# Performance work log

Hardware: AMD Instinct MI355X
Metric: run time of the kernel (lower is better)

The kernel has to match this reference:

```python
import jax, jax.numpy as jnp
import numpy as np

NUM_EXPERTS = 16
EFF_THRESHOLD = 0.1
SIM_THRESHOLD = 0.0
EPS = 1e-8


def setup_inputs() -> dict:
    key = jax.random.key(0)
    k1, k2 = jax.random.split(key)
    B, E, H = 4096, NUM_EXPERTS, 1024
    rp = jax.random.uniform(k1, (B, E), dtype=jnp.float32)
    rp = rp / rp.sum(axis=-1, keepdims=True)  # valid probabilities
    emb = jax.random.normal(k2, (B, H), dtype=jnp.float32)
    return {"routing_probs": rp, "input_embeddings": emb}


def _total_loss(routing_probs, input_embeddings):
    B, E = routing_probs.shape

    # --- LoadBalanceLoss: var(mean usage) / (1/E)^2, unbiased var (torch default)
    usage = routing_probs.mean(axis=0)                      # [E]
    var = jnp.sum((usage - usage.mean()) ** 2) / (E - 1)
    load_balance = var * (E ** 2)

    # --- EntropyRegularizationLoss (target None): -mean entropy
    entropy = -jnp.sum(routing_probs * jnp.log(routing_probs + EPS), axis=-1)
    entropy_loss = -entropy.mean()

    # --- EfficiencyLoss: sum of probs below threshold, averaged over batch
    small = jnp.where(routing_probs < EFF_THRESHOLD, routing_probs, 0.0)
    efficiency = small.sum(axis=-1).mean()

    # --- ConsistencyLoss: mean KL(softmax(p_j) || softmax(p_i)) over similar pairs
    logp = jax.nn.log_softmax(routing_probs, axis=-1)       # [B, E]
    q = jnp.exp(logp)                                       # [B, E]
    neg_ent_q = jnp.sum(q * logp, axis=-1)                  # [B], = sum q log q
    # KL[i, j] = sum_e q_j (log q_j - logp_i) = neg_ent_q[j] - logp_i . q_j
    kl = neg_ent_q[None, :] - jnp.einsum('ie,je->ij', logp, q)  # [B, B]

    nemb = input_embeddings / jnp.linalg.norm(input_embeddings, axis=-1, keepdims=True)
    sim = nemb @ nemb.T                                     # [B, B]
    mask = (sim > SIM_THRESHOLD) & (~jnp.eye(B, dtype=bool))
    num_pairs = mask.sum()
    cons_sum = jnp.sum(jnp.where(mask, kl, 0.0))
    consistency = jnp.where(num_pairs > 0,
                            cons_sum / jnp.maximum(num_pairs, 1).astype(kl.dtype),
                            0.0)

    return load_balance + entropy_loss + efficiency + consistency


def reference(routing_probs, input_embeddings):
    return _total_loss(routing_probs, input_embeddings)
```

## Files before the change

kernel.cpp:

```cpp
#include <hip/hip_runtime.h>
#include <hip/hip_bf16.h>

#define BROWS 4096
#define NE    16
#define HDIM  1024
#define ACC_F 128
#define NTILE 32
#define NBLK  (NTILE * (NTILE + 1) / 2)

typedef __attribute__((ext_vector_type(8))) short short8;
typedef __attribute__((ext_vector_type(4))) float float4v;
typedef __attribute__((ext_vector_type(2))) long long2v;

__device__ __forceinline__ unsigned bf16rne(float f) {
    const unsigned u = __float_as_uint(f);
    return (u + 0x7FFFu + ((u >> 16) & 1u)) >> 16;
}
__device__ __forceinline__ unsigned pk2(float lo, float hi) {
    return bf16rne(lo) | (bf16rne(hi) << 16);
}

__device__ __forceinline__ unsigned e4m3(float x) {
    unsigned u = __float_as_uint(x);
    const unsigned s = (u >> 24) & 0x80u;
    u &= 0x7FFFFFFFu;
    if (u >= 0x43E80000u) return s | 0x7Eu;
    u += 0x7FFFFu + ((u >> 20) & 1u);
    const int e = (int)(u >> 23) - 120;
    if (e <= 0) return s;
    return s | ((unsigned)e << 3) | ((u >> 20) & 7u);
}

__device__ __forceinline__ void gl16(const unsigned char* g, unsigned char* l) {
    __builtin_amdgcn_global_load_lds(
        (const __attribute__((address_space(1))) unsigned int*)(unsigned long long)g,
        (__attribute__((address_space(3))) unsigned int*)(unsigned int)(unsigned long long)l,
        16, 0, 0);
}

__device__ __forceinline__ void row16f(const float* src, float* p) {
    const float4v* pv = (const float4v*)src;
    float4v a0 = pv[0], a1 = pv[1], a2 = pv[2], a3 = pv[3];
    p[0]=a0.x; p[1]=a0.y; p[2]=a0.z; p[3]=a0.w;
    p[4]=a1.x; p[5]=a1.y; p[6]=a1.z; p[7]=a1.w;
    p[8]=a2.x; p[9]=a2.y; p[10]=a2.z; p[11]=a2.w;
    p[12]=a3.x; p[13]=a3.y; p[14]=a3.z; p[15]=a3.w;
}

__device__ __forceinline__ void lsm16(const float* p, float* lp, float* q, float& ne) {
    float m = p[0];
#pragma unroll
    for (int e = 1; e < 16; e++) m = fmaxf(m, p[e]);
    float s = 0.f;
#pragma unroll
    for (int e = 0; e < 16; e++) s += expf(p[e] - m);
    const float ls = logf(s);
    ne = 0.f;
#pragma unroll
    for (int e = 0; e < 16; e++) {
        lp[e] = p[e] - m - ls;
        q[e]  = expf(lp[e]);
        ne   += q[e] * lp[e];
    }
}

__device__ __forceinline__ void st8pair(unsigned char* tile, int row, int cp, uint4 v) {
    const int x = row & 7;
    unsigned long long lo = ((unsigned long long)v.y << 32) | v.x;
    unsigned long long hi = ((unsigned long long)v.w << 32) | v.z;
    *(unsigned long long*)(tile + row * 64 + (((2 * cp)     ^ x) << 3)) = lo;
    *(unsigned long long*)(tile + row * 64 + (((2 * cp + 1) ^ x) << 3)) = hi;
}

__global__ __launch_bounds__(256) void conv_init(
    const float* __restrict__ src, unsigned char* __restrict__ dst, float* __restrict__ acc)
{
    if (blockIdx.x == 0 && threadIdx.x < ACC_F) acc[threadIdx.x] = 0.f;
    const size_t k = ((size_t)blockIdx.x * 256 + threadIdx.x) * 8;
    const size_t row = k >> 10;
    const int kin = (int)(k & 1023);
    const int T = kin >> 6, kt = kin & 63, s = kt >> 5, u = (kt & 31) >> 3;
    float4v a = *(const float4v*)(src + k);
    float4v b = *(const float4v*)(src + k + 4);
    unsigned lo = e4m3(a.x) | (e4m3(a.y) << 8) | (e4m3(a.z) << 16) | (e4m3(a.w) << 24);
    unsigned hi = e4m3(b.x) | (e4m3(b.y) << 8) | (e4m3(b.z) << 16) | (e4m3(b.w) << 24);
    *(unsigned long long*)(dst + row * 1024 + T * 64 + u * 16 + s * 8) =
        ((unsigned long long)hi << 32) | lo;
}

__device__ __forceinline__ void decode_pair(int id, int& bi, int& bj) {
    int L = (id & 7) * 66 + (id >> 3);
    int gi = 0, gj = 0;
    for (;;) {
        const int cnt = (gi == gj) ? 10 : 16;
        if (L < cnt) break;
        L -= cnt;
        gj++; if (gj == 8) { gi++; gj = gi; }
    }
    if (gi == gj) {
        int u = 0, c = 4;
        while (L >= c) { L -= c; u++; c--; }
        bi = gi * 4 + u; bj = gj * 4 + u + L;
    } else {
        bi = gi * 4 + (L >> 2); bj = gj * 4 + (L & 3);
    }
}

template<bool PRE>
__global__ __launch_bounds__(512, 4) void gram_kl(
    const float* __restrict__ embf, const unsigned char* __restrict__ embq,
    const float* __restrict__ rp, float* __restrict__ acc,
    unsigned int* __restrict__ out)
{
    __shared__ char smem[32768];
    __shared__ float red[16];
    __shared__ int islast;
    __shared__ float fin[96];
    __hip_bfloat16* eAF = (__hip_bfloat16*)smem;
    __hip_bfloat16* eBF = (__hip_bfloat16*)(smem + 8192);
    __hip_bfloat16* eAR = (__hip_bfloat16*)(smem + 16384);
    __hip_bfloat16* eBR = (__hip_bfloat16*)(smem + 24576);

    int bi, bj;
    decode_pair((int)blockIdx.x, bi, bj);

    const int t = threadIdx.x;
    const int lane = t & 63, wid = t >> 6;
    const int wi0 = (wid >> 1) * 32, wj0 = (wid & 1) * 64;
    const int lrow = lane & 15, quad = lane >> 4;

    float4v accf[2][4];
#pragma unroll
    for (int a = 0; a < 2; a++)
#pragma unroll
        for (int b = 0; b < 4; b++) { accf[a][b].x=0.f; accf[a][b].y=0.f; accf[a][b].z=0.f; accf[a][b].w=0.f; }

    if (PRE) {
        int roA[2], roB[4];
#pragma unroll
        for (int f = 0; f < 2; f++) {
            const int r = wi0 + f * 16 + lrow;
            roA[f] = r * 64 + ((quad ^ ((r >> 1) & 3)) << 4);
        }
#pragma unroll
        for (int f = 0; f < 4; f++) {
            const int r = wj0 + f * 16 + lrow;
            roB[f] = r * 64 + ((quad ^ ((r >> 1) & 3)) << 4);
        }
        const int rl = lane >> 2;
        const int r  = wid * 16 + rl;
        const int gu = (lane & 3) ^ ((r >> 1) & 3);
        const unsigned char* gA = embq + (size_t)(bi * 128 + r) * 1024 + gu * 16;
        const unsigned char* gB = embq + (size_t)(bj * 128 + r) * 1024 + gu * 16;
        const int woff = wid * 1024;

        gl16(gA, (unsigned char*)smem + woff);
        gl16(gB, (unsigned char*)smem + 8192 + woff);
        for (int T = 0; T < 16; ++T) {
            unsigned char* cur = (unsigned char*)smem + (T & 1) * 16384;
            unsigned char* nxt = (unsigned char*)smem + ((T + 1) & 1) * 16384;
            __syncthreads();
            if (T < 15) {
                const int kt = (T + 1) * 64;
                gl16(gA + kt, nxt + woff);
                gl16(gB + kt, nxt + 8192 + woff);
            }
            long2v A0 = *(const long2v*)(cur + roA[0]);
            long2v A1 = *(const long2v*)(cur + roA[1]);
            long2v B0 = *(const long2v*)(cur + 8192 + roB[0]);
            long2v B1 = *(const long2v*)(cur + 8192 + roB[1]);
            long2v B2 = *(const long2v*)(cur + 8192 + roB[2]);
            long2v B3 = *(const long2v*)(cur + 8192 + roB[3]);
            accf[0][0] = __builtin_amdgcn_mfma_f32_16x16x32_fp8_fp8(A0.x, B0.x, accf[0][0], 0, 0, 0);
            accf[0][1] = __builtin_amdgcn_mfma_f32_16x16x32_fp8_fp8(A0.x, B1.x, accf[0][1], 0, 0, 0);
            accf[0][2] = __builtin_amdgcn_mfma_f32_16x16x32_fp8_fp8(A0.x, B2.x, accf[0][2], 0, 0, 0);
            accf[0][3] = __builtin_amdgcn_mfma_f32_16x16x32_fp8_fp8(A0.x, B3.x, accf[0][3], 0, 0, 0);
            accf[1][0] = __builtin_amdgcn_mfma_f32_16x16x32_fp8_fp8(A1.x, B0.x, accf[1][0], 0, 0, 0);
            accf[1][1] = __builtin_amdgcn_mfma_f32_16x16x32_fp8_fp8(A1.x, B1.x, accf[1][1], 0, 0, 0);
            accf[1][2] = __builtin_amdgcn_mfma_f32_16x16x32_fp8_fp8(A1.x, B2.x, accf[1][2], 0, 0, 0);
            accf[1][3] = __builtin_amdgcn_mfma_f32_16x16x32_fp8_fp8(A1.x, B3.x, accf[1][3], 0, 0, 0);
            accf[0][0] = __builtin_amdgcn_mfma_f32_16x16x32_fp8_fp8(A0.y, B0.y, accf[0][0], 0, 0, 0);
            accf[0][1] = __builtin_amdgcn_mfma_f32_16x16x32_fp8_fp8(A0.y, B1.y, accf[0][1], 0, 0, 0);
            accf[0][2] = __builtin_amdgcn_mfma_f32_16x16x32_fp8_fp8(A0.y, B2.y, accf[0][2], 0, 0, 0);
            accf[0][3] = __builtin_amdgcn_mfma_f32_16x16x32_fp8_fp8(A0.y, B3.y, accf[0][3], 0, 0, 0);
            accf[1][0] = __builtin_amdgcn_mfma_f32_16x16x32_fp8_fp8(A1.y, B0.y, accf[1][0], 0, 0, 0);
            accf[1][1] = __builtin_amdgcn_mfma_f32_16x16x32_fp8_fp8(A1.y, B1.y, accf[1][1], 0, 0, 0);
            accf[1][2] = __builtin_amdgcn_mfma_f32_16x16x32_fp8_fp8(A1.y, B2.y, accf[1][2], 0, 0, 0);
            accf[1][3] = __builtin_amdgcn_mfma_f32_16x16x32_fp8_fp8(A1.y, B3.y, accf[1][3], 0, 0, 0);
        }
    } else {
        int roA[2][2], roB[4][2];
#pragma unroll
        for (int f = 0; f < 2; f++) {
            const int r = wi0 + f * 16 + lrow;
#pragma unroll
            for (int s = 0; s < 2; s++) roA[f][s] = r * 64 + (((s * 4 + quad) ^ (r & 7)) << 3);
        }
#pragma unroll
        for (int f = 0; f < 4; f++) {
            const int r = wj0 + f * 16 + lrow;
#pragma unroll
            for (int s = 0; s < 2; s++) roB[f][s] = r * 64 + (((s * 4 + quad) ^ (r & 7)) << 3);
        }
        const int row = t >> 2, cp = t & 3;
        const float* gA = embf + (size_t)(bi * 128 + row) * HDIM + cp * 16;
        const float* gB = embf + (size_t)(bj * 128 + row) * HDIM + cp * 16;
        for (int T = 0; T < 16; ++T) {
            const int kt = T * 64;
            unsigned char* bufA = (unsigned char*)(smem + (T & 1) * 16384);
            unsigned char* bufB = bufA + 8192;
            uint4 wa, wb;
            {
                float4v x0 = *(const float4v*)(gA + kt),      x1 = *(const float4v*)(gA + kt + 4);
                float4v x2 = *(const float4v*)(gA + kt + 8),  x3 = *(const float4v*)(gA + kt + 12);
                wa.x = e4m3(x0.x) | (e4m3(x0.y)<<8) | (e4m3(x0.z)<<16) | (e4m3(x0.w)<<24);
                wa.y = e4m3(x1.x) | (e4m3(x1.y)<<8) | (e4m3(x1.z)<<16) | (e4m3(x1.w)<<24);
                wa.z = e4m3(x2.x) | (e4m3(x2.y)<<8) | (e4m3(x2.z)<<16) | (e4m3(x2.w)<<24);
                wa.w = e4m3(x3.x) | (e4m3(x3.y)<<8) | (e4m3(x3.z)<<16) | (e4m3(x3.w)<<24);
                float4v y0 = *(const float4v*)(gB + kt),      y1 = *(const float4v*)(gB + kt + 4);
                float4v y2 = *(const float4v*)(gB + kt + 8),  y3 = *(const float4v*)(gB + kt + 12);
                wb.x = e4m3(y0.x) | (e4m3(y0.y)<<8) | (e4m3(y0.z)<<16) | (e4m3(y0.w)<<24);
                wb.y = e4m3(y1.x) | (e4m3(y1.y)<<8) | (e4m3(y1.z)<<16) | (e4m3(y1.w)<<24);
                wb.z = e4m3(y2.x) | (e4m3(y2.y)<<8) | (e4m3(y2.z)<<16) | (e4m3(y2.w)<<24);
                wb.w = e4m3(y3.x) | (e4m3(y3.y)<<8) | (e4m3(y3.z)<<16) | (e4m3(y3.w)<<24);
            }
            st8pair(bufA, row, cp, wa);
            st8pair(bufB, row, cp, wb);
            __syncthreads();
#pragma unroll
            for (int s = 0; s < 2; s++) {
                long a0 = *(const long*)(bufA + roA[0][s]);
                long a1 = *(const long*)(bufA + roA[1][s]);
                long b0 = *(const long*)(bufB + roB[0][s]);
                long b1 = *(const long*)(bufB + roB[1][s]);
                long b2 = *(const long*)(bufB + roB[2][s]);
                long b3 = *(const long*)(bufB + roB[3][s]);
                accf[0][0] = __builtin_amdgcn_mfma_f32_16x16x32_fp8_fp8(a0, b0, accf[0][0], 0, 0, 0);
                accf[0][1] = __builtin_amdgcn_mfma_f32_16x16x32_fp8_fp8(a0, b1, accf[0][1], 0, 0, 0);
                accf[0][2] = __builtin_amdgcn_mfma_f32_16x16x32_fp8_fp8(a0, b2, accf[0][2], 0, 0, 0);
                accf[0][3] = __builtin_amdgcn_mfma_f32_16x16x32_fp8_fp8(a0, b3, accf[0][3], 0, 0, 0);
                accf[1][0] = __builtin_amdgcn_mfma_f32_16x16x32_fp8_fp8(a1, b0, accf[1][0], 0, 0, 0);
                accf[1][1] = __builtin_amdgcn_mfma_f32_16x16x32_fp8_fp8(a1, b1, accf[1][1], 0, 0, 0);
                accf[1][2] = __builtin_amdgcn_mfma_f32_16x16x32_fp8_fp8(a1, b2, accf[1][2], 0, 0, 0);
                accf[1][3] = __builtin_amdgcn_mfma_f32_16x16x32_fp8_fp8(a1, b3, accf[1][3], 0, 0, 0);
            }
            __syncthreads();
        }
    }
    __syncthreads();

    {
        float p[16], lp[16], q[16], ne;
        const bool iSide = (t < 128);
        if (t < 256) {
            const int rloc = iSide ? t : (t - 128);
            const int grow = (iSide ? bi : bj) * 128 + rloc;
            row16f(rp + (size_t)grow * NE, p);
            lsm16(p, lp, q, ne);
            float r1[16], r2[16], x1, x2;
            if (iSide) {
#pragma unroll
                for (int e = 0; e < 16; e++) { r1[e] = lp[e]; r2[e] = q[e]; }
                x1 = 1.f; x2 = ne;
            } else {
#pragma unroll
                for (int e = 0; e < 16; e++) { r1[e] = -q[e]; r2[e] = -lp[e]; }
                x1 = ne; x2 = 1.f;
            }
            const int s = (rloc >> 1) & 3;
            __hip_bfloat16* d1 = (iSide ? eAF : eBF) + rloc * 32;
            __hip_bfloat16* d2 = (iSide ? eAR : eBR) + rloc * 32;
            uint4 w0 = {pk2(r1[0],r1[1]), pk2(r1[2],r1[3]), pk2(r1[4],r1[5]), pk2(r1[6],r1[7])};
            uint4 w1 = {pk2(r1[8],r1[9]), pk2(r1[10],r1[11]), pk2(r1[12],r1[13]), pk2(r1[14],r1[15])};
            uint4 w2 = {pk2(x1, 0.f), 0u, 0u, 0u};
            uint4 w3 = {0u, 0u, 0u, 0u};
            *(uint4*)(d1 + (0 ^ s) * 8) = w0;
            *(uint4*)(d1 + (1 ^ s) * 8) = w1;
            *(uint4*)(d1 + (2 ^ s) * 8) = w2;
            *(uint4*)(d1 + (3 ^ s) * 8) = w3;
            uint4 v0 = {pk2(r2[0],r2[1]), pk2(r2[2],r2[3]), pk2(r2[4],r2[5]), pk2(r2[6],r2[7])};
            uint4 v1 = {pk2(r2[8],r2[9]), pk2(r2[10],r2[11]), pk2(r2[12],r2[13]), pk2(r2[14],r2[15])};
            uint4 v2 = {pk2(x2, 0.f), 0u, 0u, 0u};
            *(uint4*)(d2 + (0 ^ s) * 8) = v0;
            *(uint4*)(d2 + (1 ^ s) * 8) = v1;
            *(uint4*)(d2 + (2 ^ s) * 8) = v2;
            *(uint4*)(d2 + (3 ^ s) * 8) = w3;
        }
        if (bi == bj && iSide) {
            float ent = 0.f, eff = 0.f;
#pragma unroll
            for (int e = 0; e < 16; e++) {
                ent += p[e] * logf(p[e] + 1e-8f);
                if (p[e] < 0.1f) eff += p[e];
            }
#pragma unroll
            for (int e = 0; e < 18; e++) {
                float v = (e < 16) ? p[e] : ((e == 16) ? ent : eff);
#pragma unroll
                for (int o = 32; o > 0; o >>= 1) v += __shfl_down(v, o);
                if (lane == 0) atomicAdd(&acc[e], v);
            }
        }
    }
    __syncthreads();

    int eoA[2], eoB[4];
#pragma unroll
    for (int f = 0; f < 2; f++) {
        const int r = wi0 + f * 16 + lrow;
        eoA[f] = r * 32 + (quad ^ ((r >> 1) & 3)) * 8;
    }
#pragma unroll
    for (int f = 0; f < 4; f++) {
        const int r = wj0 + f * 16 + lrow;
        eoB[f] = r * 32 + (quad ^ ((r >> 1) & 3)) * 8;
    }

    float4v accF[2][4], accR[2][4];
    {
        const float4v z = {0.f, 0.f, 0.f, 0.f};
        short8 af[2], ar[2], bfr[4], brr[4];
#pragma unroll
        for (int f = 0; f < 2; f++) {
            af[f] = *(const short8*)(eAF + eoA[f]);
            ar[f] = *(const short8*)(eAR + eoA[f]);
        }
#pragma unroll
        for (int f = 0; f < 4; f++) {
            bfr[f] = *(const short8*)(eBF + eoB[f]);
            brr[f] = *(const short8*)(eBR + eoB[f]);
        }
#pragma unroll
        for (int fi = 0; fi < 2; fi++)
#pragma unroll
            for (int fj = 0; fj < 4; fj++) {
                accF[fi][fj] = __builtin_amdgcn_mfma_f32_16x16x32_bf16(af[fi], bfr[fj], z, 0, 0, 0);
                accR[fi][fj] = __builtin_amdgcn_mfma_f32_16x16x32_bf16(ar[fi], brr[fj], z, 0, 0, 0);
            }
    }

    float klacc = 0.f, cntacc = 0.f;
    const bool offd = (bi != bj);
#pragma unroll
    for (int fi = 0; fi < 2; fi++) {
#pragma unroll
        for (int fj = 0; fj < 4; fj++) {
#pragma unroll
            for (int rg = 0; rg < 4; rg++) {
                const int ig = bi * 128 + wi0 + fi * 16 + quad * 4 + rg;
                const int jg = bj * 128 + wj0 + fj * 16 + lrow;
                const float g = accf[fi][fj][rg];
                if ((g > 0.f) && (ig != jg)) {
                    klacc  += accF[fi][fj][rg];
                    cntacc += 1.f;
                    if (offd) { klacc += accR[fi][fj][rg]; cntacc += 1.f; }
                }
            }
        }
    }

#pragma unroll
    for (int o = 32; o > 0; o >>= 1) {
        klacc  += __shfl_down(klacc, o);
        cntacc += __shfl_down(cntacc, o);
    }
    if (lane == 0) { red[wid] = klacc; red[8 + wid] = cntacc; }
    __syncthreads();
    if (t == 0) {
        float k = 0.f, c = 0.f;
#pragma unroll
        for (int w = 0; w < 8; w++) { k += red[w]; c += red[8 + w]; }
        atomicAdd(&acc[18 + ((int)blockIdx.x & 31)], k);
        atomicAdd(&acc[50 + ((int)blockIdx.x & 31)], c);
        const unsigned got = __hip_atomic_fetch_add((unsigned int*)(acc + 82), 1u,
                                                    __ATOMIC_RELEASE, __HIP_MEMORY_SCOPE_AGENT);
        islast = (got == NBLK - 1) ? 1 : 0;
    }
    __syncthreads();

    if (islast) {
        if (t == 0)
            (void)__hip_atomic_load((unsigned int*)(acc + 82), __ATOMIC_ACQUIRE,
                                    __HIP_MEMORY_SCOPE_AGENT);
        __syncthreads();
        if (t < 82)
            fin[t] = __hip_atomic_load(&acc[t], __ATOMIC_RELAXED, __HIP_MEMORY_SCOPE_AGENT);
        __syncthreads();
        if (t == 0) {
            float u[16], usum = 0.f;
#pragma unroll
            for (int e = 0; e < 16; e++) { u[e] = fin[e] / (float)BROWS; usum += u[e]; }
            const float mean = usum / 16.f;
            float var = 0.f;
#pragma unroll
            for (int e = 0; e < 16; e++) { float dd = u[e] - mean; var += dd * dd; }
            var /= 15.f;
            const float lb  = var * 256.f;
            const float ent = fin[16] / (float)BROWS;
            const float eff = fin[17] / (float)BROWS;
            float kl = 0.f, cnt = 0.f;
#pragma unroll
            for (int s = 0; s < 32; s++) { kl += fin[18 + s]; cnt += fin[50 + s]; }
            const float cons = (cnt > 0.f) ? (kl / fmaxf(cnt, 1.f)) : 0.f;
            const float total = lb + ent + eff + cons;
            const unsigned fb   = __float_as_uint(total);
            const unsigned hi   = fb >> 16;
            const unsigned mant = fb & 0xFFFFu;
            const unsigned rnd  = (mant > 0x8000u || (mant == 0x8000u && (hi & 1))) ? 1u : 0u;
            out[0] = (fb & 0xFFFF0000u) | ((hi + rnd) & 0xFFFFu);
        }
    }
}

extern "C" void kernel_launch(void* const* d_in, const int* in_sizes, int n_in,
                              void* d_out, int out_size, void* d_ws, size_t ws_size,
                              hipStream_t stream) {
    const float* rp  = (const float*)d_in[0];
    const float* emb = (const float*)d_in[1];
    float* acc = (float*)d_ws;
    unsigned char* embq = (unsigned char*)d_ws + ACC_F * sizeof(float);
    (void)in_sizes; (void)n_in; (void)out_size;

    const size_t need = ACC_F * sizeof(float) + (size_t)BROWS * HDIM;
    const bool pre = (ws_size >= need);

    if (pre) {
        conv_init<<<(BROWS * HDIM) / (256 * 8), 256, 0, stream>>>(emb, embq, acc);
        gram_kl<true><<<NBLK, 512, 0, stream>>>(emb, embq, rp, acc, (unsigned int*)d_out);
    } else {
        conv_init<<<1, 256, 0, stream>>>(emb, embq, acc);
        gram_kl<false><<<NBLK, 512, 0, stream>>>(emb, (const unsigned char*)nullptr, rp, acc,
                                                 (unsigned int*)d_out);
    }
}
```

Measured before the change: 106.7 us.

## Use 32x32x64 scaled FP8 MFMA and precompute routing log-softmax planes in conv kernel

The precomputed path now runs the gram product with the 32x32x64 f8f6f4 scaled MFMA over 128-byte K chunks, which halves the loop trip count and enlarges shared-memory double buffers to 64KB. The per-row log-softmax, entropy, efficiency and usage terms are moved into extra blocks of the conversion kernel. These blocks write bf16 augmented planes and per-block partial sums, so the gram kernel only loads prepacked fragments for the KL MFMAs. The aim is fewer MFMA and loop-issue instructions and less redundant per-tile softmax work. In exchange, the larger LDS footprint may reduce occupancy, and the extra workspace needs to be available.

Result: slower. 201.7 us (+89.0%).

```diff
diff --git a/kernel.cpp b/kernel.cpp
--- a/kernel.cpp
+++ b/kernel.cpp
@@ -4,13 +4,17 @@
 #define BROWS 4096
 #define NE    16
 #define HDIM  1024
-#define ACC_F 128
+#define ACC_F 512
 #define NTILE 32
 #define NBLK  (NTILE * (NTILE + 1) / 2)
-
-typedef __attribute__((ext_vector_type(8))) short short8;
-typedef __attribute__((ext_vector_type(4))) float float4v;
-typedef __attribute__((ext_vector_type(2))) long long2v;
+#define PLANE 262144
+#define EMBQ_BYTES 4194304
+
+typedef __attribute__((ext_vector_type(8)))  short short8;
+typedef __attribute__((ext_vector_type(4)))  float float4v;
+typedef __attribute__((ext_vector_type(16))) float float16v;
+typedef __attribute__((ext_vector_type(4)))  int   int4v;
+typedef __attribute__((ext_vector_type(8)))  int   int8v;
 
 __device__ __forceinline__ unsigned bf16rne(float f) {
     const unsigned u = __float_as_uint(f);
@@ -70,22 +74,6 @@
     unsigned long long hi = ((unsigned long long)v.w << 32) | v.z;
     *(unsigned long long*)(tile + row * 64 + (((2 * cp)     ^ x) << 3)) = lo;
     *(unsigned long long*)(tile + row * 64 + (((2 * cp + 1) ^ x) << 3)) = hi;
-}
-
-__global__ __launch_bounds__(256) void conv_init(
-    const float* __restrict__ src, unsigned char* __restrict__ dst, float* __restrict__ acc)
-{
-    if (blockIdx.x == 0 && threadIdx.x < ACC_F) acc[threadIdx.x] = 0.f;
-    const size_t k = ((size_t)blockIdx.x * 256 + threadIdx.x) * 8;
-    const size_t row = k >> 10;
-    const int kin = (int)(k & 1023);
-    const int T = kin >> 6, kt = kin & 63, s = kt >> 5, u = (kt & 31) >> 3;
-    float4v a = *(const float4v*)(src + k);
-    float4v b = *(const float4v*)(src + k + 4);
-    unsigned lo = e4m3(a.x) | (e4m3(a.y) << 8) | (e4m3(a.z) << 16) | (e4m3(a.w) << 24);
-    unsigned hi = e4m3(b.x) | (e4m3(b.y) << 8) | (e4m3(b.z) << 16) | (e4m3(b.w) << 24);
-    *(unsigned long long*)(dst + row * 1024 + T * 64 + u * 16 + s * 8) =
-        ((unsigned long long)hi << 32) | lo;
 }
 
 __device__ __forceinline__ void decode_pair(int id, int& bi, int& bj) {
@@ -106,89 +94,298 @@
     }
 }
 
+__global__ __launch_bounds__(256) void conv_init(
+    const float* __restrict__ src, unsigned char* __restrict__ dst,
+    const float* __restrict__ rp, unsigned char* __restrict__ aug,
+    float* __restrict__ acc, int nconv)
+{
+    __shared__ float sred[72];
+    const int t = threadIdx.x;
+    const int bid = (int)blockIdx.x;
+    if (bid == 0 && t < 96) acc[t] = 0.f;
+    if (bid < nconv) {
+        const size_t k = ((size_t)bid * 256 + t) * 8;
+        float4v a = *(const float4v*)(src + k);
+        float4v b = *(const float4v*)(src + k + 4);
+        unsigned lo = e4m3(a.x) | (e4m3(a.y) << 8) | (e4m3(a.z) << 16) | (e4m3(a.w) << 24);
+        unsigned hi = e4m3(b.x) | (e4m3(b.y) << 8) | (e4m3(b.z) << 16) | (e4m3(b.w) << 24);
+        *(unsigned long long*)(dst + k) = ((unsigned long long)hi << 32) | lo;
+    } else if (nconv > 0) {
+        const int pb  = bid - nconv;
+        const int row = pb * 256 + t;
+        const int lane = t & 63, wid = t >> 6;
+        float p[16], lp[16], q[16], ne;
+        row16f(rp + (size_t)row * NE, p);
+        lsm16(p, lp, q, ne);
+        const uint4 z4 = {0u, 0u, 0u, 0u};
+        {
+            uint4* d = (uint4*)(aug + (size_t)row * 64);
+            uint4 w0 = {pk2(lp[0],lp[1]), pk2(lp[2],lp[3]), pk2(lp[4],lp[5]), pk2(lp[6],lp[7])};
+            uint4 w1 = {pk2(lp[8],lp[9]), pk2(lp[10],lp[11]), pk2(lp[12],lp[13]), pk2(lp[14],lp[15])};
+            uint4 w2 = {pk2(1.f, 0.f), 0u, 0u, 0u};
+            d[0] = w0; d[1] = w1; d[2] = w2; d[3] = z4;
+        }
+        {
+            uint4* d = (uint4*)(aug + PLANE + (size_t)row * 64);
+            uint4 w0 = {pk2(q[0],q[1]), pk2(q[2],q[3]), pk2(q[4],q[5]), pk2(q[6],q[7])};
+            uint4 w1 = {pk2(q[8],q[9]), pk2(q[10],q[11]), pk2(q[12],q[13]), pk2(q[14],q[15])};
+            uint4 w2 = {pk2(ne, 0.f), 0u, 0u, 0u};
+            d[0] = w0; d[1] = w1; d[2] = w2; d[3] = z4;
+        }
+        {
+            uint4* d = (uint4*)(aug + 2 * PLANE + (size_t)row * 64);
+            uint4 w0 = {pk2(-q[0],-q[1]), pk2(-q[2],-q[3]), pk2(-q[4],-q[5]), pk2(-q[6],-q[7])};
+            uint4 w1 = {pk2(-q[8],-q[9]), pk2(-q[10],-q[11]), pk2(-q[12],-q[13]), pk2(-q[14],-q[15])};
+            uint4 w2 = {pk2(ne, 0.f), 0u, 0u, 0u};
+            d[0] = w0; d[1] = w1; d[2] = w2; d[3] = z4;
+        }
+        {
+            uint4* d = (uint4*)(aug + 3 * PLANE + (size_t)row * 64);
+            uint4 w0 = {pk2(-lp[0],-lp[1]), pk2(-lp[2],-lp[3]), pk2(-lp[4],-lp[5]), pk2(-lp[6],-lp[7])};
+            uint4 w1 = {pk2(-lp[8],-lp[9]), pk2(-lp[10],-lp[11]), pk2(-lp[12],-lp[13]), pk2(-lp[14],-lp[15])};
+            uint4 w2 = {pk2(1.f, 0.f), 0u, 0u, 0u};
+            d[0] = w0; d[1] = w1; d[2] = w2; d[3] = z4;
+        }
+        float ent = 0.f, eff = 0.f;
+#pragma unroll
+        for (int e = 0; e < 16; e++) {
+            ent += p[e] * logf(p[e] + 1e-8f);
+            if (p[e] < 0.1f) eff += p[e];
+        }
+        float vals[18];
+#pragma unroll
+        for (int e = 0; e < 16; e++) vals[e] = p[e];
+        vals[16] = ent; vals[17] = eff;
+#pragma unroll
+        for (int e = 0; e < 18; e++) {
+#pragma unroll
+            for (int o = 32; o > 0; o >>= 1) vals[e] += __shfl_down(vals[e], o);
+        }
+        if (lane == 0) {
+#pragma unroll
+            for (int e = 0; e < 18; e++) sred[wid * 18 + e] = vals[e];
+        }
+        __syncthreads();
+        if (t < 18)
+            acc[96 + pb * 18 + t] = sred[t] + sred[18 + t] + sred[36 + t] + sred[54 + t];
+    }
+}
+
 template<bool PRE>
 __global__ __launch_bounds__(512, 4) void gram_kl(
     const float* __restrict__ embf, const unsigned char* __restrict__ embq,
-    const float* __restrict__ rp, float* __restrict__ acc,
-    unsigned int* __restrict__ out)
+    const float* __restrict__ rp, const unsigned char* __restrict__ aug,
+    float* __restrict__ acc, unsigned int* __restrict__ out)
 {
-    __shared__ char smem[32768];
-    __shared__ float red[16];
-    __shared__ int islast;
-    __shared__ float fin[96];
-    __hip_bfloat16* eAF = (__hip_bfloat16*)smem;
-    __hip_bfloat16* eBF = (__hip_bfloat16*)(smem + 8192);
-    __hip_bfloat16* eAR = (__hip_bfloat16*)(smem + 16384);
-    __hip_bfloat16* eBR = (__hip_bfloat16*)(smem + 24576);
-
+    __shared__ char smem[65536];
     int bi, bj;
     decode_pair((int)blockIdx.x, bi, bj);
-
     const int t = threadIdx.x;
     const int lane = t & 63, wid = t >> 6;
     const int wi0 = (wid >> 1) * 32, wj0 = (wid & 1) * 64;
-    const int lrow = lane & 15, quad = lane >> 4;
-
-    float4v accf[2][4];
-#pragma unroll
-    for (int a = 0; a < 2; a++)
-#pragma unroll
-        for (int b = 0; b < 4; b++) { accf[a][b].x=0.f; accf[a][b].y=0.f; accf[a][b].z=0.f; accf[a][b].w=0.f; }
-
-    if (PRE) {
-        int roA[2], roB[4];
-#pragma unroll
-        for (int f = 0; f < 2; f++) {
-            const int r = wi0 + f * 16 + lrow;
-            roA[f] = r * 64 + ((quad ^ ((r >> 1) & 3)) << 4);
-        }
-#pragma unroll
-        for (int f = 0; f < 4; f++) {
-            const int r = wj0 + f * 16 + lrow;
-            roB[f] = r * 64 + ((quad ^ ((r >> 1) & 3)) << 4);
-        }
-        const int rl = lane >> 2;
-        const int r  = wid * 16 + rl;
-        const int gu = (lane & 3) ^ ((r >> 1) & 3);
-        const unsigned char* gA = embq + (size_t)(bi * 128 + r) * 1024 + gu * 16;
-        const unsigned char* gB = embq + (size_t)(bj * 128 + r) * 1024 + gu * 16;
-        const int woff = wid * 1024;
-
-        gl16(gA, (unsigned char*)smem + woff);
-        gl16(gB, (unsigned char*)smem + 8192 + woff);
-        for (int T = 0; T < 16; ++T) {
-            unsigned char* cur = (unsigned char*)smem + (T & 1) * 16384;
-            unsigned char* nxt = (unsigned char*)smem + ((T + 1) & 1) * 16384;
+
+    if constexpr (PRE) {
+        const int l31 = lane & 31, lhi = lane >> 5;
+        float16v accG[2];
+#pragma unroll
+        for (int jt = 0; jt < 2; ++jt)
+#pragma unroll
+            for (int r = 0; r < 16; ++r) accG[jt][r] = 0.f;
+
+        int roA[2][2], roB[2][2][2];
+        {
+            const int rA = wi0 + l31;
+#pragma unroll
+            for (int c = 0; c < 2; ++c)
+#pragma unroll
+                for (int e = 0; e < 2; ++e) {
+                    const int u = c * 4 + lhi * 2 + e;
+                    roA[c][e] = rA * 128 + ((u ^ (rA & 7)) << 4);
+                }
+#pragma unroll
+            for (int jt = 0; jt < 2; ++jt) {
+                const int rB = wj0 + jt * 32 + l31;
+#pragma unroll
+                for (int c = 0; c < 2; ++c)
+#pragma unroll
+                    for (int e = 0; e < 2; ++e) {
+                        const int u = c * 4 + lhi * 2 + e;
+                        roB[jt][c][e] = rB * 128 + ((u ^ (rB & 7)) << 4);
+                    }
+            }
+        }
+        const unsigned char* gA[2];
+        const unsigned char* gB[2];
+        int ldoff[2];
+        {
+            const int rg0 = lane >> 3, pu = lane & 7;
+#pragma unroll
+            for (int c8 = 0; c8 < 2; ++c8) {
+                const int rr = wid * 16 + c8 * 8 + rg0;
+                const int gu = pu ^ (rr & 7);
+                gA[c8] = embq + (size_t)(bi * 128 + rr) * 1024 + (gu << 4);
+                gB[c8] = embq + (size_t)(bj * 128 + rr) * 1024 + (gu << 4);
+                ldoff[c8] = (wid * 16 + c8 * 8) * 128;
+            }
+        }
+        {
+            unsigned char* b0 = (unsigned char*)smem;
+            gl16(gA[0], b0 + ldoff[0]);
+            gl16(gA[1], b0 + ldoff[1]);
+            gl16(gB[0], b0 + 16384 + ldoff[0]);
+            gl16(gB[1], b0 + 16384 + ldoff[1]);
+        }
+        for (int T = 0; T < 8; ++T) {
+            unsigned char* cur = (unsigned char*)smem + (T & 1) * 32768;
+            unsigned char* nxt = (unsigned char*)smem + ((T + 1) & 1) * 32768;
             __syncthreads();
-            if (T < 15) {
-                const int kt = (T + 1) * 64;
-                gl16(gA + kt, nxt + woff);
-                gl16(gB + kt, nxt + 8192 + woff);
-            }
-            long2v A0 = *(const long2v*)(cur + roA[0]);
-            long2v A1 = *(const long2v*)(cur + roA[1]);
-            long2v B0 = *(const long2v*)(cur + 8192 + roB[0]);
-            long2v B1 = *(const long2v*)(cur + 8192 + roB[1]);
-            long2v B2 = *(const long2v*)(cur + 8192 + roB[2]);
-            long2v B3 = *(const long2v*)(cur + 8192 + roB[3]);
-            accf[0][0] = __builtin_amdgcn_mfma_f32_16x16x32_fp8_fp8(A0.x, B0.x, accf[0][0], 0, 0, 0);
-            accf[0][1] = __builtin_amdgcn_mfma_f32_16x16x32_fp8_fp8(A0.x, B1.x, accf[0][1], 0, 0, 0);
-            accf[0][2] = __builtin_amdgcn_mfma_f32_16x16x32_fp8_fp8(A0.x, B2.x, accf[0][2], 0, 0, 0);
-            accf[0][3] = __builtin_amdgcn_mfma_f32_16x16x32_fp8_fp8(A0.x, B3.x, accf[0][3], 0, 0, 0);
-            accf[1][0] = __builtin_amdgcn_mfma_f32_16x16x32_fp8_fp8(A1.x, B0.x, accf[1][0], 0, 0, 0);
-            accf[1][1] = __builtin_amdgcn_mfma_f32_16x16x32_fp8_fp8(A1.x, B1.x, accf[1][1], 0, 0, 0);
-            accf[1][2] = __builtin_amdgcn_mfma_f32_16x16x32_fp8_fp8(A1.x, B2.x, accf[1][2], 0, 0, 0);
-            accf[1][3] = __builtin_amdgcn_mfma_f32_16x16x32_fp8_fp8(A1.x, B3.x, accf[1][3], 0, 0, 0);
-            accf[0][0] = __builtin_amdgcn_mfma_f32_16x16x32_fp8_fp8(A0.y, B0.y, accf[0][0], 0, 0, 0);
-            accf[0][1] = __builtin_amdgcn_mfma_f32_16x16x32_fp8_fp8(A0.y, B1.y, accf[0][1], 0, 0, 0);
-            accf[0][2] = __builtin_amdgcn_mfma_f32_16x16x32_fp8_fp8(A0.y, B2.y, accf[0][2], 0, 0, 0);
-            accf[0][3] = __builtin_amdgcn_mfma_f32_16x16x32_fp8_fp8(A0.y, B3.y, accf[0][3], 0, 0, 0);
-            accf[1][0] = __builtin_amdgcn_mfma_f32_16x16x32_fp8_fp8(A1.y, B0.y, accf[1][0], 0, 0, 0);
-            accf[1][1] = __builtin_amdgcn_mfma_f32_16x16x32_fp8_fp8(A1.y, B1.y, accf[1][1], 0, 0, 0);
-            accf[1][2] = __builtin_amdgcn_mfma_f32_16x16x32_fp8_fp8(A1.y, B2.y, accf[1][2], 0, 0, 0);
-            accf[1][3] = __builtin_amdgcn_mfma_f32_16x16x32_fp8_fp8(A1.y, B3.y, accf[1][3], 0, 0, 0);
+            if (T < 7) {
+                const int kt = (T + 1) * 128;
+                gl16(gA[0] + kt, nxt + ldoff[0]);
+                gl16(gA[1] + kt, nxt + ldoff[1]);
+                gl16(gB[0] + kt, nxt + 16384 + ldoff[0]);
+                gl16(gB[1] + kt, nxt + 16384 + ldoff[1]);
+            }
+            unsigned char* curB = cur + 16384;
+#pragma unroll
+            for (int c = 0; c < 2; ++c) {
+                int4v a0 = *(const int4v*)(cur + roA[c][0]);
+                int4v a1 = *(const int4v*)(cur + roA[c][1]);
+                int8v A = __builtin_shufflevector(a0, a1, 0, 1, 2, 3, 4, 5, 6, 7);
+#pragma unroll
+                for (int jt = 0; jt < 2; ++jt) {
+                    int4v b0 = *(const int4v*)(curB + roB[jt][c][0]);
+                    int4v b1 = *(const int4v*)(curB + roB[jt][c][1]);
+                    int8v B = __builtin_shufflevector(b0, b1, 0, 1, 2, 3, 4, 5, 6, 7);
+                    accG[jt] = __builtin_amdgcn_mfma_scale_f32_32x32x64_f8f6f4(
+                        A, B, accG[jt], 0, 0, 0, 0x7F7F7F7F, 0, 0x7F7F7F7F);
+                }
+            }
+        }
+        __syncthreads();
+
+        const unsigned char* AFp = aug;
+        const unsigned char* ARp = aug + PLANE;
+        const unsigned char* BFp = aug + 2 * PLANE;
+        const unsigned char* BRp = aug + 3 * PLANE;
+        short8 af[2], ar[2];
+        {
+            const size_t ra = (size_t)(bi * 128 + wi0 + l31) * 64 + (size_t)(lhi << 4);
+            af[0] = *(const short8*)(AFp + ra);
+            af[1] = *(const short8*)(AFp + ra + 32);
+            ar[0] = *(const short8*)(ARp + ra);
+            ar[1] = *(const short8*)(ARp + ra + 32);
+        }
+        float klacc = 0.f, cntacc = 0.f;
+        const bool offd = (bi != bj);
+#pragma unroll
+        for (int jt = 0; jt < 2; ++jt) {
+            const int jg = bj * 128 + wj0 + jt * 32 + l31;
+            const size_t rb = (size_t)jg * 64 + (size_t)(lhi << 4);
+            short8 bfr0 = *(const short8*)(BFp + rb);
+            short8 bfr1 = *(const short8*)(BFp + rb + 32);
+            short8 brr0 = *(const short8*)(BRp + rb);
+            short8 brr1 = *(const short8*)(BRp + rb + 32);
+            float16v zz;
+#pragma unroll
+            for (int r = 0; r < 16; ++r) zz[r] = 0.f;
+            float16v aF = __builtin_amdgcn_mfma_f32_32x32x16_bf16(af[0], bfr0, zz, 0, 0, 0);
+            aF = __builtin_amdgcn_mfma_f32_32x32x16_bf16(af[1], bfr1, aF, 0, 0, 0);
+            float16v aR = __builtin_amdgcn_mfma_f32_32x32x16_bf16(ar[0], brr0, zz, 0, 0, 0);
+            aR = __builtin_amdgcn_mfma_f32_32x32x16_bf16(ar[1], brr1, aR, 0, 0, 0);
+#pragma unroll
+            for (int r = 0; r < 16; ++r) {
+                const int ig = bi * 128 + wi0 + (r & 3) + 8 * (r >> 2) + 4 * lhi;
+                const float g = accG[jt][r];
+                if ((g > 0.f) && (ig != jg)) {
+                    klacc  += aF[r];
+                    cntacc += 1.f;
+                    if (offd) { klacc += aR[r]; cntacc += 1.f; }
+                }
+            }
+        }
+
+#pragma unroll
+        for (int o = 32; o > 0; o >>= 1) {
+            klacc  += __shfl_down(klacc, o);
+            cntacc += __shfl_down(cntacc, o);
+        }
+        float* red = (float*)smem;
+        float* F1  = (float*)(smem + 256);
+        float* F2  = (float*)(smem + 512);
+        int*  pisl = (int*)(smem + 2048);
+        if (lane == 0) { red[wid] = klacc; red[8 + wid] = cntacc; }
+        __syncthreads();
+        if (t == 0) {
+            float k = 0.f, c = 0.f;
+#pragma unroll
+            for (int w = 0; w < 8; w++) { k += red[w]; c += red[8 + w]; }
+            atomicAdd(&acc[18 + ((int)blockIdx.x & 31)], k);
+            atomicAdd(&acc[50 + ((int)blockIdx.x & 31)], c);
+            const unsigned got = __hip_atomic_fetch_add((unsigned int*)(acc + 82), 1u,
+                                                        __ATOMIC_RELEASE, __HIP_MEMORY_SCOPE_AGENT);
+            pisl[0] = (got == NBLK - 1) ? 1 : 0;
+        }
+        __syncthreads();
+
+        if (pisl[0]) {
+            if (t == 0)
+                (void)__hip_atomic_load((unsigned int*)(acc + 82), __ATOMIC_ACQUIRE,
+                                        __HIP_MEMORY_SCOPE_AGENT);
+            __syncthreads();
+            if (t < 64)
+                F1[t] = __hip_atomic_load(&acc[18 + t], __ATOMIC_RELAXED, __HIP_MEMORY_SCOPE_AGENT);
+            if (t < 288)
+                F2[t] = __hip_atomic_load(&acc[96 + t], __ATOMIC_RELAXED, __HIP_MEMORY_SCOPE_AGENT);
+            __syncthreads();
+            if (t == 0) {
+                float u[16], usum = 0.f, ents = 0.f, effs = 0.f;
+#pragma unroll
+                for (int e = 0; e < 16; e++) u[e] = 0.f;
+                for (int b = 0; b < 16; b++) {
+#pragma unroll
+                    for (int e = 0; e < 16; e++) u[e] += F2[b * 18 + e];
+                    ents += F2[b * 18 + 16];
+                    effs += F2[b * 18 + 17];
+                }
+#pragma unroll
+                for (int e = 0; e < 16; e++) { u[e] /= (float)BROWS; usum += u[e]; }
+                const float mean = usum / 16.f;
+                float var = 0.f;
+#pragma unroll
+                for (int e = 0; e < 16; e++) { float dd = u[e] - mean; var += dd * dd; }
+                var /= 15.f;
+                const float lb  = var * 256.f;
+                const float ent = ents / (float)BROWS;
+                const float eff = effs / (float)BROWS;
+                float kl = 0.f, cnt = 0.f;
+#pragma unroll
+                for (int s = 0; s < 32; s++) { kl += F1[s]; cnt += F1[32 + s]; }
+                const float cons = (cnt > 0.f) ? (kl / fmaxf(cnt, 1.f)) : 0.f;
+                const float total = lb + ent + eff + cons;
+                const unsigned fb   = __float_as_uint(total);
+                const unsigned hi   = fb >> 16;
+                const unsigned mant = fb & 0xFFFFu;
+                const unsigned rnd  = (mant > 0x8000u || (mant == 0x8000u && (hi & 1))) ? 1u : 0u;
+                out[0] = (fb & 0xFFFF0000u) | ((hi + rnd) & 0xFFFFu);
+            }
         }
     } else {
+        __hip_bfloat16* eAF = (__hip_bfloat16*)smem;
+        __hip_bfloat16* eBF = (__hip_bfloat16*)(smem + 8192);
+        __hip_bfloat16* eAR = (__hip_bfloat16*)(smem + 16384);
+        __hip_bfloat16* eBR = (__hip_bfloat16*)(smem + 24576);
+        float* red  = (float*)(smem + 40960);
+        int*   pisl = (int*)(smem + 41024);
+        float* fin  = (float*)(smem + 41088);
+        const int lrow = lane & 15, quad = lane >> 4;
+
+        float4v accf[2][4];
+#pragma unroll
+        for (int a = 0; a < 2; a++)
+#pragma unroll
+            for (int b = 0; b < 4; b++) { accf[a][b].x=0.f; accf[a][b].y=0.f; accf[a][b].z=0.f; accf[a][b].w=0.f; }
+
         int roA[2][2], roB[4][2];
 #pragma unroll
         for (int f = 0; f < 2; f++) {
@@ -246,168 +443,168 @@
             }
             __syncthreads();
         }
-    }
-    __syncthreads();
-
-    {
-        float p[16], lp[16], q[16], ne;
-        const bool iSide = (t < 128);
-        if (t < 256) {
-            const int rloc = iSide ? t : (t - 128);
-            const int grow = (iSide ? bi : bj) * 128 + rloc;
-            row16f(rp + (size_t)grow * NE, p);
-            lsm16(p, lp, q, ne);
-            float r1[16], r2[16], x1, x2;
-            if (iSide) {
-#pragma unroll
-                for (int e = 0; e < 16; e++) { r1[e] = lp[e]; r2[e] = q[e]; }
-                x1 = 1.f; x2 = ne;
-            } else {
-#pragma unroll
-                for (int e = 0; e < 16; e++) { r1[e] = -q[e]; r2[e] = -lp[e]; }
-                x1 = ne; x2 = 1.f;
-            }
-            const int s = (rloc >> 1) & 3;
-            __hip_bfloat16* d1 = (iSide ? eAF : eBF) + rloc * 32;
-            __hip_bfloat16* d2 = (iSide ? eAR : eBR) + rloc * 32;
-            uint4 w0 = {pk2(r1[0],r1[1]), pk2(r1[2],r1[3]), pk2(r1[4],r1[5]), pk2(r1[6],r1[7])};
-            uint4 w1 = {pk2(r1[8],r1[9]), pk2(r1[10],r1[11]), pk2(r1[12],r1[13]), pk2(r1[14],r1[15])};
-            uint4 w2 = {pk2(x1, 0.f), 0u, 0u, 0u};
-            uint4 w3 = {0u, 0u, 0u, 0u};
-            *(uint4*)(d1 + (0 ^ s) * 8) = w0;
-            *(uint4*)(d1 + (1 ^ s) * 8) = w1;
-            *(uint4*)(d1 + (2 ^ s) * 8) = w2;
-            *(uint4*)(d1 + (3 ^ s) * 8) = w3;
-            uint4 v0 = {pk2(r2[0],r2[1]), pk2(r2[2],r2[3]), pk2(r2[4],r2[5]), pk2(r2[6],r2[7])};
-            uint4 v1 = {pk2(r2[8],r2[9]), pk2(r2[10],r2[11]), pk2(r2[12],r2[13]), pk2(r2[14],r2[15])};
-            uint4 v2 = {pk2(x2, 0.f), 0u, 0u, 0u};
-            *(uint4*)(d2 + (0 ^ s) * 8) = v0;
-            *(uint4*)(d2 + (1 ^ s) * 8) = v1;
-            *(uint4*)(d2 + (2 ^ s) * 8) = v2;
-            *(uint4*)(d2 + (3 ^ s) * 8) = w3;
-        }
-        if (bi == bj && iSide) {
-            float ent = 0.f, eff = 0.f;
-#pragma unroll
-            for (int e = 0; e < 16; e++) {
-                ent += p[e] * logf(p[e] + 1e-8f);
-                if (p[e] < 0.1f) eff += p[e];
-            }
-#pragma unroll
-            for (int e = 0; e < 18; e++) {
-                float v = (e < 16) ? p[e] : ((e == 16) ? ent : eff);
-#pragma unroll
-                for (int o = 32; o > 0; o >>= 1) v += __shfl_down(v, o);
-                if (lane == 0) atomicAdd(&acc[e], v);
-            }
-        }
-    }
-    __syncthreads();
-
-    int eoA[2], eoB[4];
-#pragma unroll
-    for (int f = 0; f < 2; f++) {
-        const int r = wi0 + f * 16 + lrow;
-        eoA[f] = r * 32 + (quad ^ ((r >> 1) & 3)) * 8;
-    }
-#pragma unroll
-    for (int f = 0; f < 4; f++) {
-        const int r = wj0 + f * 16 + lrow;
-        eoB[f] = r * 32 + (quad ^ ((r >> 1) & 3)) * 8;
-    }
-
-    float4v accF[2][4], accR[2][4];
-    {
-        const float4v z = {0.f, 0.f, 0.f, 0.f};
-        short8 af[2], ar[2], bfr[4], brr[4];
+        __syncthreads();
+
+        {
+            float p[16], lp[16], q[16], ne;
+            const bool iSide = (t < 128);
+            if (t < 256) {
+                const int rloc = iSide ? t : (t - 128);
+                const int grow = (iSide ? bi : bj) * 128 + rloc;
+                row16f(rp + (size_t)grow * NE, p);
+                lsm16(p, lp, q, ne);
+                float r1[16], r2[16], x1, x2;
+                if (iSide) {
+#pragma unroll
+                    for (int e = 0; e < 16; e++) { r1[e] = lp[e]; r2[e] = q[e]; }
+                    x1 = 1.f; x2 = ne;
+                } else {
+#pragma unroll
+                    for (int e = 0; e < 16; e++) { r1[e] = -q[e]; r2[e] = -lp[e]; }
+                    x1 = ne; x2 = 1.f;
+                }
+                const int s = (rloc >> 1) & 3;
+                __hip_bfloat16* d1 = (iSide ? eAF : eBF) + rloc * 32;
+                __hip_bfloat16* d2 = (iSide ? eAR : eBR) + rloc * 32;
+                uint4 w0 = {pk2(r1[0],r1[1]), pk2(r1[2],r1[3]), pk2(r1[4],r1[5]), pk2(r1[6],r1[7])};
+                uint4 w1 = {pk2(r1[8],r1[9]), pk2(r1[10],r1[11]), pk2(r1[12],r1[13]), pk2(r1[14],r1[15])};
+                uint4 w2 = {pk2(x1, 0.f), 0u, 0u, 0u};
+                uint4 w3 = {0u, 0u, 0u, 0u};
+                *(uint4*)(d1 + (0 ^ s) * 8) = w0;
+                *(uint4*)(d1 + (1 ^ s) * 8) = w1;
+                *(uint4*)(d1 + (2 ^ s) * 8) = w2;
+                *(uint4*)(d1 + (3 ^ s) * 8) = w3;
+                uint4 v0 = {pk2(r2[0],r2[1]), pk2(r2[2],r2[3]), pk2(r2[4],r2[5]), pk2(r2[6],r2[7])};
+                uint4 v1 = {pk2(r2[8],r2[9]), pk2(r2[10],r2[11]), pk2(r2[12],r2[13]), pk2(r2[14],r2[15])};
+                uint4 v2 = {pk2(x2, 0.f), 0u, 0u, 0u};
+                *(uint4*)(d2 + (0 ^ s) * 8) = v0;
+                *(uint4*)(d2 + (1 ^ s) * 8) = v1;
+                *(uint4*)(d2 + (2 ^ s) * 8) = v2;
+                *(uint4*)(d2 + (3 ^ s) * 8) = w3;
+            }
+            if (bi == bj && iSide) {
+                float ent = 0.f, eff = 0.f;
+#pragma unroll
+                for (int e = 0; e < 16; e++) {
+                    ent += p[e] * logf(p[e] + 1e-8f);
+                    if (p[e] < 0.1f) eff += p[e];
+                }
+#pragma unroll
+                for (int e = 0; e < 18; e++) {
+                    float v = (e < 16) ? p[e] : ((e == 16) ? ent : eff);
+#pragma unroll
+                    for (int o = 32; o > 0; o >>= 1) v += __shfl_down(v, o);
+                    if (lane == 0) atomicAdd(&acc[e], v);
+                }
+            }
+        }
+        __syncthreads();
+
+        int eoA[2], eoB[4];
 #pragma unroll
         for (int f = 0; f < 2; f++) {
-            af[f] = *(const short8*)(eAF + eoA[f]);
-            ar[f] = *(const short8*)(eAR + eoA[f]);
+            const int r = wi0 + f * 16 + lrow;
+            eoA[f] = r * 32 + (quad ^ ((r >> 1) & 3)) * 8;
         }
 #pragma unroll
         for (int f = 0; f < 4; f++) {
-            bfr[f] = *(const short8*)(eBF + eoB[f]);
-            brr[f] = *(const short8*)(eBR + eoB[f]);
-        }
-#pragma unroll
-        for (int fi = 0; fi < 2; fi++)
+            const int r = wj0 + f * 16 + lrow;
+            eoB[f] = r * 32 + (quad ^ ((r >> 1) & 3)) * 8;
+        }
+
+        float4v accF[2][4], accR[2][4];
+        {
+            const float4v z = {0.f, 0.f, 0.f, 0.f};
+            short8 af[2], ar[2], bfr[4], brr[4];
+#pragma unroll
+            for (int f = 0; f < 2; f++) {
+                af[f] = *(const short8*)(eAF + eoA[f]);
+                ar[f] = *(const short8*)(eAR + eoA[f]);
+            }
+#pragma unroll
+            for (int f = 0; f < 4; f++) {
+                bfr[f] = *(const short8*)(eBF + eoB[f]);
+                brr[f] = *(const short8*)(eBR + eoB[f]);
+            }
+#pragma unroll
+            for (int fi = 0; fi < 2; fi++)
+#pragma unroll
+                for (int fj = 0; fj < 4; fj++) {
+                    accF[fi][fj] = __builtin_amdgcn_mfma_f32_16x16x32_bf16(af[fi], bfr[fj], z, 0, 0, 0);
+                    accR[fi][fj] = __builtin_amdgcn_mfma_f32_16x16x32_bf16(ar[fi], brr[fj], z, 0, 0, 0);
+                }
+        }
+
+        float klacc = 0.f, cntacc = 0.f;
+        const bool offd = (bi != bj);
+#pragma unroll
+        for (int fi = 0; fi < 2; fi++) {
 #pragma unroll
             for (int fj = 0; fj < 4; fj++) {
-                accF[fi][fj] = __builtin_amdgcn_mfma_f32_16x16x32_bf16(af[fi], bfr[fj], z, 0, 0, 0);
-                accR[fi][fj] = __builtin_amdgcn_mfma_f32_16x16x32_bf16(ar[fi], brr[fj], z, 0, 0, 0);
-            }
-    }
-
-    float klacc = 0.f, cntacc = 0.f;
-    const bool offd = (bi != bj);
-#pragma unroll
-    for (int fi = 0; fi < 2; fi++) {
-#pragma unroll
-        for (int fj = 0; fj < 4; fj++) {
-#pragma unroll
-            for (int rg = 0; rg < 4; rg++) {
-                const int ig = bi * 128 + wi0 + fi * 16 + quad * 4 + rg;
-                const int jg = bj * 128 + wj0 + fj * 16 + lrow;
-                const float g = accf[fi][fj][rg];
-                if ((g > 0.f) && (ig != jg)) {
-                    klacc  += accF[fi][fj][rg];
-                    cntacc += 1.f;
-                    if (offd) { klacc += accR[fi][fj][rg]; cntacc += 1.f; }
-                }
-            }
-        }
-    }
-
-#pragma unroll
-    for (int o = 32; o > 0; o >>= 1) {
-        klacc  += __shfl_down(klacc, o);
-        cntacc += __shfl_down(cntacc, o);
-    }
-    if (lane == 0) { red[wid] = klacc; red[8 + wid] = cntacc; }
-    __syncthreads();
-    if (t == 0) {
-        float k = 0.f, c = 0.f;
-#pragma unroll
-        for (int w = 0; w < 8; w++) { k += red[w]; c += red[8 + w]; }
-        atomicAdd(&acc[18 + ((int)blockIdx.x & 31)], k);
-        atomicAdd(&acc[50 + ((int)blockIdx.x & 31)], c);
-        const unsigned got = __hip_atomic_fetch_add((unsigned int*)(acc + 82), 1u,
-                                                    __ATOMIC_RELEASE, __HIP_MEMORY_SCOPE_AGENT);
-        islast = (got == NBLK - 1) ? 1 : 0;
-    }
-    __syncthreads();
-
-    if (islast) {
-        if (t == 0)
-            (void)__hip_atomic_load((unsigned int*)(acc + 82), __ATOMIC_ACQUIRE,
-                                    __HIP_MEMORY_SCOPE_AGENT);
-        __syncthreads();
-        if (t < 82)
-            fin[t] = __hip_atomic_load(&acc[t], __ATOMIC_RELAXED, __HIP_MEMORY_SCOPE_AGENT);
+#pragma unroll
+                for (int rg = 0; rg < 4; rg++) {
+                    const int ig = bi * 128 + wi0 + fi * 16 + quad * 4 + rg;
+                    const int jg = bj * 128 + wj0 + fj * 16 + lrow;
+                    const float g = accf[fi][fj][rg];
+                    if ((g > 0.f) && (ig != jg)) {
+                        klacc  += accF[fi][fj][rg];
+                        cntacc += 1.f;
+                        if (offd) { klacc += accR[fi][fj][rg]; cntacc += 1.f; }
+                    }
+                }
+            }
+        }
+
+#pragma unroll
+        for (int o = 32; o > 0; o >>= 1) {
+            klacc  += __shfl_down(klacc, o);
+            cntacc += __shfl_down(cntacc, o);
+        }
+        if (lane == 0) { red[wid] = klacc; red[8 + wid] = cntacc; }
         __syncthreads();
         if (t == 0) {
-            float u[16], usum = 0.f;
-#pragma unroll
-            for (int e = 0; e < 16; e++) { u[e] = fin[e] / (float)BROWS; usum += u[e]; }
-            const float mean = usum / 16.f;
-            float var = 0.f;
-#pragma unroll
-            for (int e = 0; e < 16; e++) { float dd = u[e] - mean; var += dd * dd; }
-            var /= 15.f;
-            const float lb  = var * 256.f;
-            const float ent = fin[16] / (float)BROWS;
-            const float eff = fin[17] / (float)BROWS;
-            float kl = 0.f, cnt = 0.f;
-#pragma unroll
-            for (int s = 0; s < 32; s++) { kl += fin[18 + s]; cnt += fin[50 + s]; }
-            const float cons = (cnt > 0.f) ? (kl / fmaxf(cnt, 1.f)) : 0.f;
-            const float total = lb + ent + eff + cons;
-            const unsigned fb   = __float_as_uint(total);
-            const unsigned hi   = fb >> 16;
-            const unsigned mant = fb & 0xFFFFu;
-            const unsigned rnd  = (mant > 0x8000u || (mant == 0x8000u && (hi & 1))) ? 1u : 0u;
-            out[0] = (fb & 0xFFFF0000u) | ((hi + rnd) & 0xFFFFu);
+            float k = 0.f, c = 0.f;
+#pragma unroll
+            for (int w = 0; w < 8; w++) { k += red[w]; c += red[8 + w]; }
+            atomicAdd(&acc[18 + ((int)blockIdx.x & 31)], k);
+            atomicAdd(&acc[50 + ((int)blockIdx.x & 31)], c);
+            const unsigned got = __hip_atomic_fetch_add((unsigned int*)(acc + 82), 1u,
+                                                        __ATOMIC_RELEASE, __HIP_MEMORY_SCOPE_AGENT);
+            pisl[0] = (got == NBLK - 1) ? 1 : 0;
+        }
+        __syncthreads();
+
+        if (pisl[0]) {
+            if (t == 0)
+                (void)__hip_atomic_load((unsigned int*)(acc + 82), __ATOMIC_ACQUIRE,
+                                        __HIP_MEMORY_SCOPE_AGENT);
+            __syncthreads();
+            if (t < 82)
+                fin[t] = __hip_atomic_load(&acc[t], __ATOMIC_RELAXED, __HIP_MEMORY_SCOPE_AGENT);
+            __syncthreads();
+            if (t == 0) {
+                float u[16], usum = 0.f;
+#pragma unroll
+                for (int e = 0; e < 16; e++) { u[e] = fin[e] / (float)BROWS; usum += u[e]; }
+                const float mean = usum / 16.f;
+                float var = 0.f;
+#pragma unroll
+                for (int e = 0; e < 16; e++) { float dd = u[e] - mean; var += dd * dd; }
+                var /= 15.f;
+                const float lb  = var * 256.f;
+                const float ent = fin[16] / (float)BROWS;
+                const float eff = fin[17] / (float)BROWS;
+                float kl = 0.f, cnt = 0.f;
+#pragma unroll
+                for (int s = 0; s < 32; s++) { kl += fin[18 + s]; cnt += fin[50 + s]; }
+                const float cons = (cnt > 0.f) ? (kl / fmaxf(cnt, 1.f)) : 0.f;
+                const float total = lb + ent + eff + cons;
+                const unsigned fb   = __float_as_uint(total);
+                const unsigned hi   = fb >> 16;
+                const unsigned mant = fb & 0xFFFFu;
+                const unsigned rnd  = (mant > 0x8000u || (mant == 0x8000u && (hi & 1))) ? 1u : 0u;
+                out[0] = (fb & 0xFFFF0000u) | ((hi + rnd) & 0xFFFFu);
+            }
         }
     }
 }
@@ -419,17 +616,19 @@
     const float* emb = (const float*)d_in[1];
     float* acc = (float*)d_ws;
     unsigned char* embq = (unsigned char*)d_ws + ACC_F * sizeof(float);
+    unsigned char* aug  = embq + EMBQ_BYTES;
     (void)in_sizes; (void)n_in; (void)out_size;
 
-    const size_t need = ACC_F * sizeof(float) + (size_t)BROWS * HDIM;
+    const size_t need = ACC_F * sizeof(float) + EMBQ_BYTES + 4 * (size_t)PLANE;
     const bool pre = (ws_size >= need);
 
     if (pre) {
-        conv_init<<<(BROWS * HDIM) / (256 * 8), 256, 0, stream>>>(emb, embq, acc);
-        gram_kl<true><<<NBLK, 512, 0, stream>>>(emb, embq, rp, acc, (unsigned int*)d_out);
+        const int nconv = (BROWS * HDIM) / (256 * 8);
+        conv_init<<<nconv + 16, 256, 0, stream>>>(emb, embq, rp, aug, acc, nconv);
+        gram_kl<true><<<NBLK, 512, 0, stream>>>(emb, embq, rp, aug, acc, (unsigned int*)d_out);
     } else {
-        conv_init<<<1, 256, 0, stream>>>(emb, embq, acc);
-        gram_kl<false><<<NBLK, 512, 0, stream>>>(emb, (const unsigned char*)nullptr, rp, acc,
+        conv_init<<<1, 256, 0, stream>>>(emb, nullptr, nullptr, nullptr, acc, 0);
+        gram_kl<false><<<NBLK, 512, 0, stream>>>(emb, nullptr, rp, nullptr, acc,
                                                  (unsigned int*)d_out);
     }
 }
```
